# Kernel tuning notes

Hardware: AMD Instinct MI355X
Metric: run time of the kernel (lower is better)

## Reference

```python
import jax, jax.numpy as jnp
import numpy as np

E4M3_MAX = 448.0
IGNORE = -1000.0
ROTARY_BASE = 10000.0


def quant_dequant_e4m3(w):
    """Emulate per-tensor FP8 E4M3 quantize->dequantize (3 mantissa bits, max 448)."""
    amax = jnp.max(jnp.abs(w))
    scale = E4M3_MAX / jnp.maximum(amax, 1e-12)
    v = w * scale
    a = jnp.abs(v)
    # exponent clipped to E4M3 range (min normal exp -6, max 8)
    e = jnp.clip(jnp.floor(jnp.log2(jnp.maximum(a, 1e-30))), -6.0, 8.0)
    step = jnp.exp2(e - 3.0)  # 3 mantissa bits
    q = jnp.clip(jnp.round(v / step) * step, -E4M3_MAX, E4M3_MAX)
    return (q / scale).astype(w.dtype)


def rotary_sin_cos(rotary_dim, n_ctx):
    pos = jnp.arange(n_ctx, dtype=jnp.float32)
    dim = jnp.arange(rotary_dim // 2, dtype=jnp.float32)
    inv_freq = ROTARY_BASE ** (-dim / (rotary_dim / 2))
    ang = pos[:, None] * inv_freq[None, :]            # [n_ctx, rotary_dim//2]
    ang = jnp.concatenate([ang, ang], axis=-1)        # [n_ctx, rotary_dim]
    return jnp.sin(ang), jnp.cos(ang)


def apply_rotary(x, sin, cos, rotary_dim):
    # x: [B, S, H, Dh]; rotate first rotary_dim dims with rotate-half convention
    S = x.shape[1]
    x_rot, x_pass = x[..., :rotary_dim], x[..., rotary_dim:]
    half = rotary_dim // 2
    x_flip = jnp.concatenate([-x_rot[..., half:], x_rot[..., :half]], axis=-1)
    c = cos[:S][None, :, None, :]
    s = sin[:S][None, :, None, :]
    out = x_rot * c + x_flip * s
    return jnp.concatenate([out, x_pass], axis=-1) if rotary_dim < x.shape[-1] else out


def setup_inputs() -> dict:
    key = jax.random.key(0)
    ks = jax.random.split(key, 8)
    B, S, D, H, Dh = 2, 2048, 1024, 16, 64
    return {
        "query_input": jax.random.normal(ks[0], (B, S, D), jnp.float32),
        "key_input": jax.random.normal(ks[1], (B, S, D), jnp.float32),
        "value_input": jax.random.normal(ks[2], (B, S, D), jnp.float32),
        "W_Q": jax.random.normal(ks[3], (H, D, Dh), jnp.float32) * 0.02,
        "W_K": jax.random.normal(ks[4], (H, D, Dh), jnp.float32) * 0.02,
        "W_V": jax.random.normal(ks[5], (H, D, Dh), jnp.float32) * 0.02,
        "W_O": jax.random.normal(ks[6], (H, Dh, D), jnp.float32) * 0.02,
        "b_Q": jnp.zeros((H, Dh), jnp.float32),
        "b_K": jnp.zeros((H, Dh), jnp.float32),
        "b_V": jnp.zeros((H, Dh), jnp.float32),
        "b_O": jnp.zeros((D,), jnp.float32),
    }


def reference(query_input, key_input, value_input, W_Q, W_K, W_V, W_O, b_Q, b_K, b_V, b_O):
    B, S, D = query_input.shape
    H, _, Dh = W_Q.shape
    rotary_dim = Dh
    attn_scale = jnp.sqrt(jnp.asarray(Dh, jnp.float32))

    # FP8-quantized QKV weights/biases (E4M3 quant-dequant emulation)
    Wq = quant_dequant_e4m3(W_Q)
    Wk = quant_dequant_e4m3(W_K)
    Wv = quant_dequant_e4m3(W_V)
    bq = quant_dequant_e4m3(b_Q)
    bk = quant_dequant_e4m3(b_K)
    bv = quant_dequant_e4m3(b_V)

    q = jnp.einsum("bsd,hde->bshe", query_input, Wq) + bq  # [B,S,H,Dh]
    k = jnp.einsum("bsd,hde->bshe", key_input, Wk) + bk
    v = jnp.einsum("bsd,hde->bshe", value_input, Wv) + bv

    sin, cos = rotary_sin_cos(rotary_dim, S)
    q = apply_rotary(q, sin, cos, rotary_dim)
    k = apply_rotary(k, sin, cos, rotary_dim)

    scores = jnp.einsum("bqhe,bkhe->bhqk", q, k) / attn_scale  # [B,H,S,S]
    causal = jnp.tril(jnp.ones((S, S), bool))
    scores = jnp.where(causal[None, None], scores, IGNORE)
    pattern = jax.nn.softmax(scores, axis=-1)

    z = jnp.einsum("bhqk,bkhe->bqhe", pattern, v)             # [B,S,H,Dh]
    out = jnp.einsum("bqhe,hed->bqd", z, W_O) + b_O           # [B,S,D]
    return out
```

## Files before the change

### kernel.cpp

```cpp
#include <hip/hip_runtime.h>
#include <math.h>


typedef __attribute__((ext_vector_type(8))) short bf16x8;
typedef __attribute__((ext_vector_type(16))) float f32x16;
typedef __attribute__((ext_vector_type(4))) float f32x4;
typedef __attribute__((ext_vector_type(4))) float f4;

#define E4M3_MAX 448.0f

__device__ inline float bf2f(ushort u) { return __uint_as_float(((unsigned)u) << 16); }
__device__ inline ushort f2bf(float f) {
  unsigned u = __float_as_uint(f);
  return (ushort)((u + 0x7FFF + ((u >> 16) & 1)) >> 16);
}
__device__ inline unsigned pack2bf(float a, float b) {
  unsigned ua = __float_as_uint(a), ub = __float_as_uint(b);
  return ((ua + 0x8000u) >> 16) | ((ub + 0x8000u) & 0xFFFF0000u);
}

__device__ __forceinline__ void gll16(const ushort* g, ushort* l) {
  __builtin_amdgcn_global_load_lds(
      (const __attribute__((address_space(1))) unsigned int*)g,
      (__attribute__((address_space(3))) unsigned int*)l, 16, 0, 0);
}

__device__ inline float qdq_qval(float w, float amax) {
  float scale = E4M3_MAX / fmaxf(amax, 1e-12f);
  float v = w * scale;
  float a = fmaxf(fabsf(v), 1e-30f);
  int ex;
  (void)frexpf(a, &ex);
  float e = fminf(fmaxf((float)(ex - 1), -6.0f), 8.0f);
  float step = exp2f(e - 3.0f);
  float q = rintf(v / step) * step;
  return fminf(fmaxf(q, -E4M3_MAX), E4M3_MAX);
}

__device__ __forceinline__ float redpart64(const float* __restrict__ p, int tid) {
  float v = p[tid & 63];
  #pragma unroll
  for (int o = 32; o > 0; o >>= 1) v = fmaxf(v, __shfl_xor(v, o));
  return v;
}

__global__ __launch_bounds__(256) void prep1(const float* __restrict__ W0,
                                             const float* __restrict__ W1,
                                             const float* __restrict__ W2,
                                             const float* __restrict__ b0,
                                             const float* __restrict__ b1,
                                             const float* __restrict__ b2,
                                             const float* __restrict__ Xq,
                                             const float* __restrict__ Xk,
                                             const float* __restrict__ Xv,
                                             float* __restrict__ amaxpart,
                                             ushort* __restrict__ xq,
                                             ushort* __restrict__ xk,
                                             ushort* __restrict__ xv) {
  __shared__ float wred[4];
  int bid = blockIdx.x, tid = threadIdx.x;
  if (bid < 384) {
    int y = bid >> 6, xb = bid & 63;
    const float* src = (y == 0) ? W0 : (y == 1) ? W1 : (y == 2) ? W2
                     : (y == 3) ? b0 : (y == 4) ? b1 : b2;
    int n = (y < 3) ? 1048576 : 1024;
    float m = 0.0f;
    for (int i = xb * 256 + tid; i < n; i += 64 * 256)
      m = fmaxf(m, fabsf(src[i]));
    #pragma unroll
    for (int off = 32; off > 0; off >>= 1)
      m = fmaxf(m, __shfl_xor(m, off));
    if ((tid & 63) == 0) wred[tid >> 6] = m;
    __syncthreads();
    if (tid == 0)
      amaxpart[y * 64 + xb] = fmaxf(fmaxf(wred[0], wred[1]), fmaxf(wred[2], wred[3]));
  } else {
    int t = bid - 384;
    int y = t >> 12, xb = t & 4095;
    const float* in = (y == 0) ? Xq : (y == 1) ? Xk : Xv;
    ushort* out = (y == 0) ? xq : (y == 1) ? xk : xv;
    int i = xb * 256 + tid;
    f4 v = *(const f4*)(in + (size_t)i * 4);
    uint2 o;
    o.x = (unsigned)f2bf(v[0]) | ((unsigned)f2bf(v[1]) << 16);
    o.y = (unsigned)f2bf(v[2]) | ((unsigned)f2bf(v[3]) << 16);
    *(uint2*)(out + (size_t)i * 4) = o;
  }
}

__global__ __launch_bounds__(256) void prep2(const float* __restrict__ W0,
                                             const float* __restrict__ W1,
                                             const float* __restrict__ W2,
                                             const float* __restrict__ WO,
                                             const float* __restrict__ b0,
                                             const float* __restrict__ b1,
                                             const float* __restrict__ b2,
                                             const float* __restrict__ amaxpart,
                                             float* __restrict__ amax,
                                             ushort* __restrict__ o0,
                                             ushort* __restrict__ o1,
                                             ushort* __restrict__ o2,
                                             ushort* __restrict__ woT,
                                             float* __restrict__ bq,
                                             float* __restrict__ bk,
                                             float* __restrict__ bv) {
  __shared__ float tile[64][65];
  int bid = blockIdx.x, tid = threadIdx.x;
  if (bid < 768) {
    int z = bid >> 8, r = bid & 255, hh = r >> 4, xb = r & 15;
    const float* W = (z == 0) ? W0 : (z == 1) ? W1 : W2;
    ushort* Bt = (z == 0) ? o0 : (z == 1) ? o1 : o2;
    float am = redpart64(amaxpart + z * 64, tid);
    if (r == 0 && tid == 0) amax[z] = am;
    int d0 = xb * 64;
    int e = tid & 63, dd = tid >> 6;
    #pragma unroll
    for (int p = 0; p < 16; p++)
      tile[dd + p * 4][e] = W[(size_t)hh * 65536 + (size_t)(d0 + dd + p * 4) * 64 + e];
    __syncthreads();
    int d = tid & 63, ee = tid >> 6;
    #pragma unroll
    for (int p = 0; p < 16; p++) {
      int e2 = ee + p * 4;
      Bt[(size_t)(hh * 64 + e2) * 1024 + d0 + d] = f2bf(qdq_qval(tile[d][e2], am));
    }
  } else if (bid < 780) {
    int q = bid - 768, y = q >> 2, xb = q & 3;
    const float* b = (y == 0) ? b0 : (y == 1) ? b1 : b2;
    float* o = (y == 0) ? bq : (y == 1) ? bk : bv;
    float am = redpart64(amaxpart + (3 + y) * 64, tid);
    int idx = xb * 256 + tid;
    if (idx < 1024) {
      float qv = qdq_qval(b[idx], am);
      o[idx] = qv * (fmaxf(am, 1e-12f) * (1.0f / E4M3_MAX));
    }
  } else {
    int t = bid - 780;
    int xb = t & 15, yb = t >> 4;
    int d0 = xb * 64, he0 = yb * 64;
    int dcol = tid & 63, hr = tid >> 6;
    #pragma unroll
    for (int p = 0; p < 16; p++)
      tile[hr + p * 4][dcol] = WO[(size_t)(he0 + hr + p * 4) * 1024 + d0 + dcol];
    __syncthreads();
    int hcol = tid & 63, dr = tid >> 6;
    #pragma unroll
    for (int p = 0; p < 16; p++)
      woT[(size_t)(d0 + dr + p * 4) * 1024 + he0 + hcol] = f2bf(tile[hcol][dr + p * 4]);
  }
}

template <int QUANT, int TN>
__device__ __forceinline__ void gemm_body(const ushort* __restrict__ A,
                                          const ushort* __restrict__ Bt,
                                          const float* __restrict__ bias, float s_inv,
                                          ushort* __restrict__ outb, float* __restrict__ outf,
                                          int bx, int by, ushort* As, ushort* Bs) {
  const int K = 1024, N = 1024;
  const int JF = TN / 32;
  int tid = threadIdx.x;
  int w = tid >> 6, lane = tid & 63, quad = lane >> 4, l16 = lane & 15;
  int wm = w & 1, wn = w >> 1;
  int row0 = by * 128, col0 = bx * TN;
  f32x4 acc[4][4] = {};

  for (int k0 = 0; k0 < K; k0 += 32) {
    __syncthreads();
    {
      int u = tid;
      gll16(&A[(size_t)(row0 + (u >> 2)) * K + k0 + (u & 3) * 8], &As[u * 8]);
      u = tid + 256;
      gll16(&A[(size_t)(row0 + (u >> 2)) * K + k0 + (u & 3) * 8], &As[u * 8]);
      u = tid;
      gll16(&Bt[(size_t)(col0 + (u >> 2)) * K + k0 + (u & 3) * 8], &Bs[u * 8]);
      if (TN == 128) {
        u = tid + 256;
        gll16(&Bt[(size_t)(col0 + (u >> 2)) * K + k0 + (u & 3) * 8], &Bs[u * 8]);
      }
    }
    __syncthreads();
    bf16x8 af[4], bfr[JF];
    #pragma unroll
    for (int i = 0; i < 4; i++)
      af[i] = *(const bf16x8*)&As[(wm * 64 + i * 16 + l16) * 32 + quad * 8];
    #pragma unroll
    for (int j = 0; j < JF; j++)
      bfr[j] = *(const bf16x8*)&Bs[(wn * (TN / 2) + j * 16 + l16) * 32 + quad * 8];
    #pragma unroll
    for (int i = 0; i < 4; i++)
      #pragma unroll
      for (int j = 0; j < JF; j++)
        acc[i][j] = __builtin_amdgcn_mfma_f32_16x16x32_bf16(af[i], bfr[j], acc[i][j], 0, 0, 0);
  }

  #pragma unroll
  for (int j = 0; j < JF; j++) {
    int col = col0 + wn * (TN / 2) + j * 16 + l16;
    float bv = bias[col];
    #pragma unroll
    for (int i = 0; i < 4; i++) {
      int row = row0 + wm * 64 + i * 16 + quad * 4;
      #pragma unroll
      for (int r = 0; r < 4; r++) {
        float v = acc[i][j][r] * s_inv + bv;
        if (QUANT) outb[(size_t)(row + r) * N + col] = f2bf(v);
        else       outf[(size_t)(row + r) * N + col] = v;
      }
    }
  }
}

__global__ __launch_bounds__(256) void gemm3_qkv(const ushort* __restrict__ xq,
                                                 const ushort* __restrict__ xk,
                                                 const ushort* __restrict__ xv,
                                                 const ushort* __restrict__ wq,
                                                 const ushort* __restrict__ wk,
                                                 const ushort* __restrict__ wv,
                                                 const float* __restrict__ bq,
                                                 const float* __restrict__ bk,
                                                 const float* __restrict__ bv,
                                                 const float* __restrict__ amax,
                                                 ushort* __restrict__ oq,
                                                 ushort* __restrict__ ok,
                                                 ushort* __restrict__ ov) {
  __shared__ ushort As[4096], Bs[4096];
  int z = blockIdx.z;
  const ushort* A  = (z == 0) ? xq : (z == 1) ? xk : xv;
  const ushort* Bt = (z == 0) ? wq : (z == 1) ? wk : wv;
  const float* bias = (z == 0) ? bq : (z == 1) ? bk : bv;
  ushort* out = (z == 0) ? oq : (z == 1) ? ok : ov;
  float s_inv = fmaxf(amax[z], 1e-12f) * (1.0f / E4M3_MAX);
  gemm_body<1, 128>(A, Bt, bias, s_inv, out, nullptr, blockIdx.x, blockIdx.y, As, Bs);
}

__global__ __launch_bounds__(256) void gemm_wo(const ushort* __restrict__ A,
                                               const ushort* __restrict__ Bt,
                                               const float* __restrict__ bias,
                                               float* __restrict__ out) {
  __shared__ ushort As[4096], Bs[2048];
  gemm_body<0, 64>(A, Bt, bias, 1.0f, nullptr, out, blockIdx.x, blockIdx.y, As, Bs);
}

__global__ __launch_bounds__(256) void rot_vtrans(ushort* __restrict__ qb,
                                                  ushort* __restrict__ kb,
                                                  const ushort* __restrict__ v,
                                                  ushort* __restrict__ vT) {
  __shared__ ushort tile[64][72];
  int bid = blockIdx.x, tid = threadIdx.x;
  if (bid < 4096) {
    int bs = bid;
    int s = bs & 2047;
    int e = tid & 63, w = tid >> 6;
    int j = e & 31;
    float inv_freq = exp2f((float)j * (-13.287712379549449f / 32.0f));
    float ang = (float)s * inv_freq;
    float c = cosf(ang), sn = sinf(ang);
    float sgn = (e < 32) ? -1.0f : 1.0f;
    size_t base = (size_t)bs * 1024;
    #pragma unroll
    for (int i = 0; i < 4; i++) {
      int h = w + i * 4;
      size_t idx = base + (size_t)h * 64 + e;
      float x = bf2f(qb[idx]);
      float xp = __shfl_xor(x, 32);
      qb[idx] = f2bf(x * c + sgn * xp * sn);
      float y = bf2f(kb[idx]);
      float yp = __shfl_xor(y, 32);
      kb[idx] = f2bf(y * c + sgn * yp * sn);
    }
  } else {
    int t = bid - 4096;
    int sx = t & 31, h = (t >> 5) & 15, b = t >> 9;
    int s0 = sx * 64;
    int e = tid & 63, sr = tid >> 6;
    #pragma unroll
    for (int p = 0; p < 16; p++)
      tile[sr + p * 4][e] = v[(size_t)(b * 2048 + s0 + sr + p * 4) * 1024 + h * 64 + e];
    __syncthreads();
    int sc = tid & 63, er = tid >> 6;
    #pragma unroll
    for (int p = 0; p < 16; p++)
      vT[(size_t)((b * 16 + h) * 64 + er + p * 4) * 2048 + s0 + sc] = tile[sc][er + p * 4];
  }
}

__global__ __launch_bounds__(512, 4) void flash_mfma9(const ushort* __restrict__ qb,
                                                      const ushort* __restrict__ kb,
                                                      const ushort* __restrict__ vT,
                                                      ushort* __restrict__ zb) {
  int h = blockIdx.y, b = blockIdx.z;
  int tid = threadIdx.x;
  int w8 = tid >> 6;
  int g = w8 >> 2;
  int w = w8 & 3;
  int lane = tid & 63, h2 = lane >> 5, l31 = lane & 31;
  __shared__ ushort sbuf[16384 + 18432];
  ushort* Ks = sbuf + g * 4096;
  ushort* Vs = sbuf + 8192 + g * 4096;
  ushort* P2 = sbuf + 16384 + g * 9216;

  const int qrow = w * 32 + l31;
  const float CE = 0.125f;

  const int ts = tid & 255;
  const int u0 = ts, u1 = ts + 256;
  const int r0 = u0 >> 3, c0 = u0 & 7, r1 = u1 >> 3, c1 = u1 & 7;
  const int sw0 = (c0 ^ (r0 & 7)) * 8, sw1 = (c1 ^ (r1 & 7)) * 8;

  const int qt = (blockIdx.z == 0) ? (int)blockIdx.x : 15 - (int)blockIdx.x;
  const int q0 = qt * 128;
  const int qg = q0 + w * 32 + l31;
  size_t qbase = ((size_t)(b * 2048 + qg)) * 1024 + (size_t)h * 64;
  bf16x8 qf[4];
  #pragma unroll
  for (int ck = 0; ck < 4; ck++)
    qf[ck] = *(const bf16x8*)&qb[qbase + ck * 16 + h2 * 8];

  f32x16 accO[2] = {};
  float mrun = -INFINITY, lrun = 0.0f;

  const int nt = qt + 1;
  const int kt0 = g * nt;

  const ushort* ksrc0 = kb + ((size_t)(b * 2048 + kt0 * 64 + r0)) * 1024 + (size_t)h * 64 + c0 * 8;
  const ushort* ksrc1 = kb + ((size_t)(b * 2048 + kt0 * 64 + r1)) * 1024 + (size_t)h * 64 + c1 * 8;
  const ushort* vsrc0 = vT + ((size_t)((b * 16 + h) * 64 + r0)) * 2048 + kt0 * 64 + c0 * 8;
  const ushort* vsrc1 = vT + ((size_t)((b * 16 + h) * 64 + r1)) * 2048 + kt0 * 64 + c1 * 8;

  uint4 kc0 = *(const uint4*)ksrc0;
  uint4 kc1 = *(const uint4*)ksrc1;
  uint4 vc0 = *(const uint4*)vsrc0;
  uint4 vc1 = *(const uint4*)vsrc1;

  for (int t = 0; t < nt; t++) {
    int kt = kt0 + t;
    __syncthreads();
    *(uint4*)&Ks[r0 * 64 + sw0] = kc0;
    *(uint4*)&Ks[r1 * 64 + sw1] = kc1;
    *(uint4*)&Vs[r0 * 64 + sw0] = vc0;
    *(uint4*)&Vs[r1 * 64 + sw1] = vc1;
    __syncthreads();
    if (t + 1 < nt) {
      kc0 = *(const uint4*)(ksrc0 + (size_t)(t + 1) * 65536);
      kc1 = *(const uint4*)(ksrc1 + (size_t)(t + 1) * 65536);
      vc0 = *(const uint4*)(vsrc0 + (t + 1) * 64);
      vc1 = *(const uint4*)(vsrc1 + (t + 1) * 64);
    }

    bool active = (kt * 64 <= q0 + w * 32 + 31);
    if (active) {
      f32x16 sc[2] = {};
      #pragma unroll
      for (int mf = 0; mf < 2; mf++) {
        int row = mf * 32 + l31;
        int s8 = row & 7;
        #pragma unroll
        for (int ck = 0; ck < 4; ck++) {
          bf16x8 ka = *(const bf16x8*)&Ks[row * 64 + (((2 * ck + h2) ^ s8) * 8)];
          sc[mf] = __builtin_amdgcn_mfma_f32_32x32x16_bf16(ka, qf[ck], sc[mf], 0, 0, 0);
        }
      }

      if (kt * 64 + 63 > q0 + w * 32) {
        #pragma unroll
        for (int mf = 0; mf < 2; mf++)
          #pragma unroll
          for (int i = 0; i < 16; i++) {
            int kv = kt * 64 + mf * 32 + (i & 3) + 8 * (i >> 2) + 4 * h2;
            sc[mf][i] = (kv > qg) ? -8000.0f : sc[mf][i];
          }
      }

      float tm = sc[0][0];
      #pragma unroll
      for (int i = 1; i < 16; i++) tm = fmaxf(tm, sc[0][i]);
      #pragma unroll
      for (int i = 0; i < 16; i++) tm = fmaxf(tm, sc[1][i]);
      tm = fmaxf(tm, __shfl_xor(tm, 32));
      float mnew = fmaxf(mrun, tm);
      float alpha = __expf((mrun - mnew) * CE);
      float p[2][16];
      float rs = 0.0f;
      #pragma unroll
      for (int mf = 0; mf < 2; mf++)
        #pragma unroll
        for (int i = 0; i < 16; i++) {
          float pv = __expf((sc[mf][i] - mnew) * CE);
          p[mf][i] = pv;
          rs += pv;
        }
      rs += __shfl_xor(rs, 32);
      lrun = lrun * alpha + rs;
      mrun = mnew;
      #pragma unroll
      for (int mf = 0; mf < 2; mf++)
        #pragma unroll
        for (int i = 0; i < 16; i++) accO[mf][i] *= alpha;

      #pragma unroll
      for (int mf = 0; mf < 2; mf++)
        #pragma unroll
        for (int m = 0; m < 4; m++) {
          uint2 w2;
          w2.x = pack2bf(p[mf][4 * m + 0], p[mf][4 * m + 1]);
          w2.y = pack2bf(p[mf][4 * m + 2], p[mf][4 * m + 3]);
          *(uint2*)&P2[qrow * 72 + 32 * mf + 8 * m + 4 * h2] = w2;
        }

      #pragma unroll
      for (int ck = 0; ck < 4; ck++) {
        bf16x8 pB = *(const bf16x8*)&P2[qrow * 72 + ck * 16 + h2 * 8];
        #pragma unroll
        for (int mf = 0; mf < 2; mf++) {
          int row = mf * 32 + l31;
          bf16x8 va = *(const bf16x8*)&Vs[row * 64 + (((2 * ck + h2) ^ (row & 7)) * 8)];
          accO[mf] = __builtin_amdgcn_mfma_f32_32x32x16_bf16(va, pB, accO[mf], 0, 0, 0);
        }
      }
    }
  }

  __syncthreads();
  float* mbuf = (float*)sbuf;
  int midx = (w * 64 + lane) * 35;
  if (g == 1) {
    #pragma unroll
    for (int i = 0; i < 16; i++) mbuf[midx + i] = accO[0][i];
    #pragma unroll
    for (int i = 0; i < 16; i++) mbuf[midx + 16 + i] = accO[1][i];
    mbuf[midx + 32] = mrun;
    mbuf[midx + 33] = lrun;
  }
  __syncthreads();
  ushort* Osb = sbuf + 16384 + 9216;
  if (g == 0) {
    float m1 = mbuf[midx + 32], l1 = mbuf[midx + 33];
    float mn = fmaxf(mrun, m1);
    float a0 = __expf((mrun - mn) * CE), a1 = __expf((m1 - mn) * CE);
    float linv = 1.0f / (lrun * a0 + l1 * a1);
    #pragma unroll
    for (int mf = 0; mf < 2; mf++)
      #pragma unroll
      for (int m = 0; m < 4; m++) {
        int e0 = 32 * mf + 8 * m + 4 * h2;
        float o0 = (accO[mf][4 * m + 0] * a0 + mbuf[midx + 16 * mf + 4 * m + 0] * a1) * linv;
        float o1 = (accO[mf][4 * m + 1] * a0 + mbuf[midx + 16 * mf + 4 * m + 1] * a1) * linv;
        float o2 = (accO[mf][4 * m + 2] * a0 + mbuf[midx + 16 * mf + 4 * m + 2] * a1) * linv;
        float o3 = (accO[mf][4 * m + 3] * a0 + mbuf[midx + 16 * mf + 4 * m + 3] * a1) * linv;
        *(unsigned*)&Osb[qrow * 72 + e0] = pack2bf(o0, o1);
        *(unsigned*)&Osb[qrow * 72 + e0 + 2] = pack2bf(o2, o3);
      }
  }
  __syncthreads();
  size_t obase = ((size_t)(b * 2048 + q0)) * 1024 + (size_t)h * 64;
  #pragma unroll
  for (int i = 0; i < 2; i++) {
    int u = tid + i * 512;
    int r = u >> 3, blk = u & 7;
    *(uint4*)&zb[obase + (size_t)r * 1024 + blk * 8] = *(const uint4*)&Osb[r * 72 + blk * 8];
  }
}

extern "C" void kernel_launch(void* const* d_in, const int* in_sizes, int n_in,
                              void* d_out, int out_size, void* d_ws, size_t ws_size,
                              hipStream_t stream) {
  const float* Xq  = (const float*)d_in[0];
  const float* Xk  = (const float*)d_in[1];
  const float* Xv  = (const float*)d_in[2];
  const float* W_Q = (const float*)d_in[3];
  const float* W_K = (const float*)d_in[4];
  const float* W_V = (const float*)d_in[5];
  const float* W_O = (const float*)d_in[6];
  const float* b_Q = (const float*)d_in[7];
  const float* b_K = (const float*)d_in[8];
  const float* b_V = (const float*)d_in[9];
  const float* b_O = (const float*)d_in[10];
  float* out = (float*)d_out;

  char* base = (char*)d_ws;
  float*  amax = (float*)(base + 0);
  float*  amaxpart = (float*)(base + 1024);
  float*  bq   = (float*)(base + 4096);
  float*  bk   = (float*)(base + 8192);
  float*  bv   = (float*)(base + 12288);
  ushort* wq   = (ushort*)(base + 16384);
  ushort* wk   = (ushort*)(base + 16384 + 2097152);
  ushort* wv   = (ushort*)(base + 16384 + 2u * 2097152);
  ushort* woT  = (ushort*)(base + 16384 + 3u * 2097152);
  ushort* xq   = (ushort*)(base + 8404992);
  ushort* xk   = (ushort*)(base + 16793600);
  ushort* xv   = (ushort*)(base + 25182208);
  ushort* qbf  = (ushort*)(base + 33570816);
  ushort* kbf  = (ushort*)(base + 41959424);
  ushort* vbf  = (ushort*)(base + 50348032);
  ushort* vT   = xq;
  ushort* zbf  = xk;

  prep1<<<12672, 256, 0, stream>>>(W_Q, W_K, W_V, b_Q, b_K, b_V, Xq, Xk, Xv,
                                   amaxpart, xq, xk, xv);
  prep2<<<1036, 256, 0, stream>>>(W_Q, W_K, W_V, W_O, b_Q, b_K, b_V,
                                  amaxpart, amax, wq, wk, wv, woT, bq, bk, bv);
  dim3 g3(8, 32, 3);
  gemm3_qkv<<<g3, 256, 0, stream>>>(xq, xk, xv, wq, wk, wv, bq, bk, bv, amax,
                                    qbf, kbf, vbf);
  rot_vtrans<<<5120, 256, 0, stream>>>(qbf, kbf, vbf, vT);
  dim3 fgrid(16, 16, 2);
  flash_mfma9<<<fgrid, 512, 0, stream>>>(qbf, kbf, vT, zbf);
  dim3 wog(16, 32);
  gemm_wo<<<wog, 256, 0, stream>>>(zbf, woT, b_O, out);
}
```

Baseline: 242.8 us.

## Fuse rotary embedding into QKV GEMM epilogue and double GEMM K-step

```diff
diff --git a/kernel.cpp b/kernel.cpp
--- a/kernel.cpp
+++ b/kernel.cpp
@@ -155,7 +155,7 @@
                                           const ushort* __restrict__ Bt,
                                           const float* __restrict__ bias, float s_inv,
                                           ushort* __restrict__ outb, float* __restrict__ outf,
-                                          int bx, int by, ushort* As, ushort* Bs) {
+                                          int bx, int by, ushort* As, ushort* Bs, int rot) {
   const int K = 1024, N = 1024;
   const int JF = TN / 32;
   int tid = threadIdx.x;
@@ -164,47 +164,74 @@
   int row0 = by * 128, col0 = bx * TN;
   f32x4 acc[4][4] = {};
 
-  for (int k0 = 0; k0 < K; k0 += 32) {
+  for (int k0 = 0; k0 < K; k0 += 64) {
     __syncthreads();
     {
-      int u = tid;
-      gll16(&A[(size_t)(row0 + (u >> 2)) * K + k0 + (u & 3) * 8], &As[u * 8]);
-      u = tid + 256;
-      gll16(&A[(size_t)(row0 + (u >> 2)) * K + k0 + (u & 3) * 8], &As[u * 8]);
-      u = tid;
-      gll16(&Bt[(size_t)(col0 + (u >> 2)) * K + k0 + (u & 3) * 8], &Bs[u * 8]);
-      if (TN == 128) {
-        u = tid + 256;
-        gll16(&Bt[(size_t)(col0 + (u >> 2)) * K + k0 + (u & 3) * 8], &Bs[u * 8]);
-      }
-    }
-    __syncthreads();
-    bf16x8 af[4], bfr[JF];
-    #pragma unroll
-    for (int i = 0; i < 4; i++)
-      af[i] = *(const bf16x8*)&As[(wm * 64 + i * 16 + l16) * 32 + quad * 8];
-    #pragma unroll
-    for (int j = 0; j < JF; j++)
-      bfr[j] = *(const bf16x8*)&Bs[(wn * (TN / 2) + j * 16 + l16) * 32 + quad * 8];
-    #pragma unroll
-    for (int i = 0; i < 4; i++)
+      #pragma unroll
+      for (int p = 0; p < 4; p++) {
+        int u = tid + p * 256;
+        gll16(&A[(size_t)(row0 + (u >> 3)) * K + k0 + (u & 7) * 8], &As[u * 8]);
+      }
+      #pragma unroll
+      for (int p = 0; p < TN / 32; p++) {
+        int u = tid + p * 256;
+        gll16(&Bt[(size_t)(col0 + (u >> 3)) * K + k0 + (u & 7) * 8], &Bs[u * 8]);
+      }
+    }
+    __syncthreads();
+    #pragma unroll
+    for (int kk = 0; kk < 2; kk++) {
+      bf16x8 af[4], bfr[JF];
+      #pragma unroll
+      for (int i = 0; i < 4; i++)
+        af[i] = *(const bf16x8*)&As[(wm * 64 + i * 16 + l16) * 64 + kk * 32 + quad * 8];
       #pragma unroll
       for (int j = 0; j < JF; j++)
-        acc[i][j] = __builtin_amdgcn_mfma_f32_16x16x32_bf16(af[i], bfr[j], acc[i][j], 0, 0, 0);
-  }
-
-  #pragma unroll
-  for (int j = 0; j < JF; j++) {
-    int col = col0 + wn * (TN / 2) + j * 16 + l16;
-    float bv = bias[col];
-    #pragma unroll
-    for (int i = 0; i < 4; i++) {
-      int row = row0 + wm * 64 + i * 16 + quad * 4;
-      #pragma unroll
-      for (int r = 0; r < 4; r++) {
-        float v = acc[i][j][r] * s_inv + bv;
-        if (QUANT) outb[(size_t)(row + r) * N + col] = f2bf(v);
-        else       outf[(size_t)(row + r) * N + col] = v;
+        bfr[j] = *(const bf16x8*)&Bs[(wn * (TN / 2) + j * 16 + l16) * 64 + kk * 32 + quad * 8];
+      #pragma unroll
+      for (int i = 0; i < 4; i++)
+        #pragma unroll
+        for (int j = 0; j < JF; j++)
+          acc[i][j] = __builtin_amdgcn_mfma_f32_16x16x32_bf16(af[i], bfr[j], acc[i][j], 0, 0, 0);
+    }
+  }
+
+  if (QUANT && rot) {
+    float bv0[4];
+    #pragma unroll
+    for (int j = 0; j < 4; j++) bv0[j] = bias[col0 + wn * 64 + j * 16 + l16];
+    #pragma unroll
+    for (int jp = 0; jp < 2; jp++) {
+      float invf = exp2f((float)(jp * 16 + l16) * (-13.287712379549449f / 32.0f));
+      int collo = col0 + wn * 64 + jp * 16 + l16;
+      #pragma unroll
+      for (int i = 0; i < 4; i++) {
+        #pragma unroll
+        for (int r = 0; r < 4; r++) {
+          int row = row0 + wm * 64 + i * 16 + quad * 4 + r;
+          float ang = (float)(row & 2047) * invf;
+          float sn = __sinf(ang), c = __cosf(ang);
+          float lo = acc[i][jp][r] * s_inv + bv0[jp];
+          float hi = acc[i][jp + 2][r] * s_inv + bv0[jp + 2];
+          outb[(size_t)row * N + collo] = f2bf(lo * c - hi * sn);
+          outb[(size_t)row * N + collo + 32] = f2bf(hi * c + lo * sn);
+        }
+      }
+    }
+  } else {
+    #pragma unroll
+    for (int j = 0; j < JF; j++) {
+      int col = col0 + wn * (TN / 2) + j * 16 + l16;
+      float bv = bias[col];
+      #pragma unroll
+      for (int i = 0; i < 4; i++) {
+        int row = row0 + wm * 64 + i * 16 + quad * 4;
+        #pragma unroll
+        for (int r = 0; r < 4; r++) {
+          float v = acc[i][j][r] * s_inv + bv;
+          if (QUANT) outb[(size_t)(row + r) * N + col] = f2bf(v);
+          else       outf[(size_t)(row + r) * N + col] = v;
+        }
       }
     }
   }
@@ -223,65 +250,40 @@
                                                  ushort* __restrict__ oq,
                                                  ushort* __restrict__ ok,
                                                  ushort* __restrict__ ov) {
-  __shared__ ushort As[4096], Bs[4096];
+  __shared__ ushort As[8192], Bs[8192];
   int z = blockIdx.z;
   const ushort* A  = (z == 0) ? xq : (z == 1) ? xk : xv;
   const ushort* Bt = (z == 0) ? wq : (z == 1) ? wk : wv;
   const float* bias = (z == 0) ? bq : (z == 1) ? bk : bv;
   ushort* out = (z == 0) ? oq : (z == 1) ? ok : ov;
   float s_inv = fmaxf(amax[z], 1e-12f) * (1.0f / E4M3_MAX);
-  gemm_body<1, 128>(A, Bt, bias, s_inv, out, nullptr, blockIdx.x, blockIdx.y, As, Bs);
+  gemm_body<1, 128>(A, Bt, bias, s_inv, out, nullptr, blockIdx.x, blockIdx.y, As, Bs,
+                    (z < 2) ? 1 : 0);
 }
 
 __global__ __launch_bounds__(256) void gemm_wo(const ushort* __restrict__ A,
                                                const ushort* __restrict__ Bt,
                                                const float* __restrict__ bias,
                                                float* __restrict__ out) {
-  __shared__ ushort As[4096], Bs[2048];
-  gemm_body<0, 64>(A, Bt, bias, 1.0f, nullptr, out, blockIdx.x, blockIdx.y, As, Bs);
-}
-
-__global__ __launch_bounds__(256) void rot_vtrans(ushort* __restrict__ qb,
-                                                  ushort* __restrict__ kb,
-                                                  const ushort* __restrict__ v,
-                                                  ushort* __restrict__ vT) {
+  __shared__ ushort As[8192], Bs[4096];
+  gemm_body<0, 64>(A, Bt, bias, 1.0f, nullptr, out, blockIdx.x, blockIdx.y, As, Bs, 0);
+}
+
+__global__ __launch_bounds__(256) void v_trans(const ushort* __restrict__ v,
+                                               ushort* __restrict__ vT) {
   __shared__ ushort tile[64][72];
-  int bid = blockIdx.x, tid = threadIdx.x;
-  if (bid < 4096) {
-    int bs = bid;
-    int s = bs & 2047;
-    int e = tid & 63, w = tid >> 6;
-    int j = e & 31;
-    float inv_freq = exp2f((float)j * (-13.287712379549449f / 32.0f));
-    float ang = (float)s * inv_freq;
-    float c = cosf(ang), sn = sinf(ang);
-    float sgn = (e < 32) ? -1.0f : 1.0f;
-    size_t base = (size_t)bs * 1024;
-    #pragma unroll
-    for (int i = 0; i < 4; i++) {
-      int h = w + i * 4;
-      size_t idx = base + (size_t)h * 64 + e;
-      float x = bf2f(qb[idx]);
-      float xp = __shfl_xor(x, 32);
-      qb[idx] = f2bf(x * c + sgn * xp * sn);
-      float y = bf2f(kb[idx]);
-      float yp = __shfl_xor(y, 32);
-      kb[idx] = f2bf(y * c + sgn * yp * sn);
-    }
-  } else {
-    int t = bid - 4096;
-    int sx = t & 31, h = (t >> 5) & 15, b = t >> 9;
-    int s0 = sx * 64;
-    int e = tid & 63, sr = tid >> 6;
-    #pragma unroll
-    for (int p = 0; p < 16; p++)
-      tile[sr + p * 4][e] = v[(size_t)(b * 2048 + s0 + sr + p * 4) * 1024 + h * 64 + e];
-    __syncthreads();
-    int sc = tid & 63, er = tid >> 6;
-    #pragma unroll
-    for (int p = 0; p < 16; p++)
-      vT[(size_t)((b * 16 + h) * 64 + er + p * 4) * 2048 + s0 + sc] = tile[sc][er + p * 4];
-  }
+  int t = blockIdx.x, tid = threadIdx.x;
+  int sx = t & 31, h = (t >> 5) & 15, b = t >> 9;
+  int s0 = sx * 64;
+  int e = tid & 63, sr = tid >> 6;
+  #pragma unroll
+  for (int p = 0; p < 16; p++)
+    tile[sr + p * 4][e] = v[(size_t)(b * 2048 + s0 + sr + p * 4) * 1024 + h * 64 + e];
+  __syncthreads();
+  int sc = tid & 63, er = tid >> 6;
+  #pragma unroll
+  for (int p = 0; p < 16; p++)
+    vT[(size_t)((b * 16 + h) * 64 + er + p * 4) * 2048 + s0 + sc] = tile[sc][er + p * 4];
 }
 
 __global__ __launch_bounds__(512, 4) void flash_mfma9(const ushort* __restrict__ qb,
@@ -503,7 +505,7 @@
   dim3 g3(8, 32, 3);
   gemm3_qkv<<<g3, 256, 0, stream>>>(xq, xk, xv, wq, wk, wv, bq, bk, bv, amax,
                                     qbf, kbf, vbf);
-  rot_vtrans<<<5120, 256, 0, stream>>>(qbf, kbf, vbf, vT);
+  v_trans<<<1024, 256, 0, stream>>>(vbf, vT);
   dim3 fgrid(16, 16, 2);
   flash_mfma9<<<fgrid, 512, 0, stream>>>(qbf, kbf, vT, zbf);
   dim3 wog(16, 32);
```

Measured after the change: 248.9 us. +2.5%, slower.
